# Kernel tuning notes

Measured on AMD Instinct MI355X. Metric: run time of the kernel, lower is better.

## Reference

```python
import jax, jax.numpy as jnp
import numpy as np

NHEAD = 16
EPS = 1e-6

def _phi_norm(x):
    # phi = silu, then L2 normalize over last dim (torch F.normalize: x / max(||x||, eps))
    x = jax.nn.silu(x)
    n = jnp.linalg.norm(x, axis=-1, keepdims=True)
    return x / jnp.maximum(n, EPS)

def setup_inputs() -> dict:
    key = jax.random.key(0)
    k1, k2, k3 = jax.random.split(key, 3)
    B, M, N, D = 4, 1024, 2048, 1024
    q = jax.random.normal(k1, (B, M, D), dtype=jnp.float32)
    kv = jax.random.normal(k2, (B, N, D), dtype=jnp.float32)
    kv_mask = jax.random.bernoulli(k3, 0.1, (B, N))  # True = masked out
    return {"q": q, "kv": kv, "kv_mask": kv_mask}

def reference(q, kv, kv_mask):
    B, M, D = q.shape
    N = kv.shape[1]
    dh = D // NHEAD
    # [B, H, M, dh] / [B, H, N, dh]
    qh = q.reshape(B, M, NHEAD, dh).transpose(0, 2, 1, 3)
    kh = kv.reshape(B, N, NHEAD, dh).transpose(0, 2, 1, 3)
    vh = kh  # values are raw kv heads (no phi/norm)
    qh_n = _phi_norm(qh)
    kh_n = _phi_norm(kh)
    scores = jnp.einsum('bhmd,bhnd->bhmn', qh_n, kh_n) / jnp.sqrt(jnp.asarray(dh, qh_n.dtype))
    scores = jnp.where(kv_mask[:, None, None, :], -jnp.inf, scores)
    attn = jax.nn.softmax(scores.astype(jnp.float32), axis=-1).astype(scores.dtype)
    out = jnp.einsum('bhmn,bhnd->bhmd', attn, vh)
    return out.transpose(0, 2, 1, 3).reshape(B, M, D)
```

## Files before the change

### kernel.cpp

```cpp
#include <hip/hip_runtime.h>
#include <hip/hip_bf16.h>
#include <cmath>
#include <stdint.h>

#define B_ 4
#define M_ 1024
#define N_ 2048
#define D_ 1024
#define H_ 16
#define DH_ 64
#define NT 64
#define NTH 16
#define PITCH 72

typedef __bf16 bf16_t;
typedef __attribute__((ext_vector_type(8))) __bf16 bf16x8;
typedef __attribute__((ext_vector_type(16))) float f32x16;
typedef __attribute__((ext_vector_type(2))) float f32x2;

static __device__ __forceinline__ float silu_f(float x) {
  return x / (1.0f + __expf(-x));
}

static __device__ __forceinline__ unsigned pk2(float a, float b) {
  union { __bf16 h[2]; unsigned u; } p;
  p.h[0] = (__bf16)a; p.h[1] = (__bf16)b;
  return p.u;
}

static __device__ __forceinline__ void gload16(const bf16_t* g, bf16_t* l) {
  typedef __attribute__((address_space(1))) const unsigned GU;
  typedef __attribute__((address_space(3))) unsigned LU;
  __builtin_amdgcn_global_load_lds((GU*)(const unsigned*)g, (LU*)(unsigned*)l,
                                   16, 0, 0);
}

static __device__ __forceinline__ int sw23(int x) {
  return (x & ~12) | ((x & 4) << 1) | ((x & 8) >> 1);
}

__global__ __launch_bounds__(256) void prep_kernel(
    const float* __restrict__ kv, const int* __restrict__ kv_mask,
    bf16_t* __restrict__ kp, bf16_t* __restrict__ vt,
    unsigned long long* __restrict__ mb) {
  __shared__ __align__(16) bf16_t Lt[NT][PITCH];
  const int bx = blockIdx.x;
  const int hp = bx & 7;
  const int nt = (bx >> 3) & 31;
  const int b  = bx >> 8;
  const int n0 = nt * NT;
  const int tid = threadIdx.x;
  const float keep = kv_mask[b * N_ + n0 + (tid >> 2)] ? 0.f : 1.f;

  #pragma unroll
  for (int hi = 0; hi < 2; ++hi) {
    const int h = hp * 2 + hi;
    const size_t bh = (size_t)(b * H_ + h);
    {
      const int r = tid >> 2, c0 = (tid & 3) * 16;
      const float* src = kv + ((size_t)(b * N_ + n0 + r)) * D_ + h * DH_ + c0;
      union { float f[16]; float4 v4[4]; } raw;
      raw.v4[0] = *(const float4*)(src + 0);
      raw.v4[1] = *(const float4*)(src + 4);
      raw.v4[2] = *(const float4*)(src + 8);
      raw.v4[3] = *(const float4*)(src + 12);
      float sv[16];
      float ss = 0.f;
      #pragma unroll
      for (int i = 0; i < 16; ++i) { sv[i] = silu_f(raw.f[i]); ss += sv[i] * sv[i]; }
      ss += __shfl_xor(ss, 1); ss += __shfl_xor(ss, 2);
      const float inv = keep / fmaxf(sqrtf(ss), 1e-6f);
      union { bf16_t bs[16]; uint4 u[2]; } pk;
      #pragma unroll
      for (int i = 0; i < 16; ++i) pk.bs[i] = (bf16_t)(sv[i] * inv);
      uint4* kdst = (uint4*)(kp + (bh * N_ + n0 + r) * DH_ + c0);
      kdst[0] = pk.u[0]; kdst[1] = pk.u[1];
      union { bf16_t bs[16]; uint4 u[2]; } pv;
      #pragma unroll
      for (int i = 0; i < 16; ++i) pv.bs[i] = (bf16_t)(raw.f[i] * keep);
      uint4* ldst = (uint4*)&Lt[r][c0];
      ldst[0] = pv.u[0]; ldst[1] = pv.u[1];
    }
    __syncthreads();
    {
      const int d = tid >> 2, nc = (tid & 3) * 16;
      union { bf16_t bs[16]; uint4 u[2]; } pk;
      #pragma unroll
      for (int i = 0; i < 16; ++i) pk.bs[i] = Lt[nc + i][d];
      uint4* dst = (uint4*)(vt + (bh * DH_ + d) * N_ + n0 + nc);
      dst[0] = pk.u[0]; dst[1] = pk.u[1];
    }
    __syncthreads();
  }
  if (bx == 0 && tid < B_ * (N_ / 64)) {
    const int b2 = tid >> 5, tt = tid & 31;
    unsigned long long m = 0ull;
    for (int i = 0; i < 64; ++i)
      if (kv_mask[b2 * N_ + tt * 64 + i]) m |= (1ull << i);
    mb[tid] = m;
  }
}

__global__ __launch_bounds__(512, 4) void attn_kernel(
    const float* __restrict__ q, const bf16_t* __restrict__ kp,
    const bf16_t* __restrict__ vt, const unsigned long long* __restrict__ mb,
    float* __restrict__ out) {
  __shared__ __align__(1024) char smem[65536];

  const int tid  = threadIdx.x;
  const int w    = tid >> 6;
  const int wq   = w & 3;
  const int half = w >> 2;
  const int lane = tid & 63;
  const int l31  = lane & 31;
  const int hi   = lane >> 5;
  const int rho  = l31 & 7;

  const int wg = (blockIdx.x & 7) * 64 + (blockIdx.x >> 3);
  const int bh = wg >> 3;
  const int m0 = (wg & 7) * 128;
  const int b = bh >> 4, h = bh & 15;

  const bf16_t* kpb = kp + (size_t)bh * N_ * DH_ + (size_t)half * NTH * NT * DH_;
  const bf16_t* vtb = vt + (size_t)bh * DH_ * N_;

  const int srow  = lane >> 3;
  const int sslot = (lane & 7) ^ srow;
  const bf16_t* ks0 = kpb + (size_t)sw23(wq * 16 + srow) * DH_ + sslot * 8;
  const bf16_t* ks1 = kpb + (size_t)sw23(wq * 16 + 8 + srow) * DH_ + sslot * 8;
  const bf16_t* vs0 = vtb + (size_t)(wq * 16 + srow) * N_ + half * NTH * NT + sslot * 8;
  const bf16_t* vs1 = vs0 + 8 * N_;

  {
    bf16_t* Kd = (bf16_t*)(smem + (half * 2 + 0) * 8192) + wq * 16 * DH_;
    bf16_t* Vd = (bf16_t*)(smem + 32768 + (half * 2 + 0) * 8192) + wq * 16 * NT;
    gload16(ks0, Kd); gload16(ks1, Kd + 512);
    gload16(vs0, Vd); gload16(vs1, Vd + 512);
  }

  bf16x8 qb[4];
  {
    const float* qrow =
        q + ((size_t)(b * M_ + m0 + wq * 32 + l31)) * D_ + h * DH_ + hi * 8;
    float sv[32];
    float ss = 0.f;
    #pragma unroll
    for (int kk = 0; kk < 4; ++kk) {
      float4 a0 = *(const float4*)(qrow + kk * 16);
      float4 a1 = *(const float4*)(qrow + kk * 16 + 4);
      sv[kk * 8 + 0] = silu_f(a0.x); sv[kk * 8 + 1] = silu_f(a0.y);
      sv[kk * 8 + 2] = silu_f(a0.z); sv[kk * 8 + 3] = silu_f(a0.w);
      sv[kk * 8 + 4] = silu_f(a1.x); sv[kk * 8 + 5] = silu_f(a1.y);
      sv[kk * 8 + 6] = silu_f(a1.z); sv[kk * 8 + 7] = silu_f(a1.w);
      #pragma unroll
      for (int i = 0; i < 8; ++i) ss += sv[kk * 8 + i] * sv[kk * 8 + i];
    }
    ss += __shfl_xor(ss, 32);
    const float inv = 0.125f / fmaxf(sqrtf(ss), 1e-6f);
    #pragma unroll
    for (int kk = 0; kk < 4; ++kk) {
      union { unsigned u[4]; bf16x8 v; } pq;
      #pragma unroll
      for (int jj = 0; jj < 4; ++jj)
        pq.u[jj] = pk2(sv[kk * 8 + jj * 2] * inv, sv[kk * 8 + jj * 2 + 1] * inv);
      qb[kk] = pq.v;
    }
  }

  int foff[2][4];
  #pragma unroll
  for (int i = 0; i < 2; ++i)
    #pragma unroll
    for (int j = 0; j < 4; ++j)
      foff[i][j] = (i * 32 + l31) * 64 + ((((j << 1) + hi) ^ rho) << 3);

  f32x16 o0, o1, zvec;
  #pragma unroll
  for (int r = 0; r < 16; ++r) { o0[r] = 0.f; o1[r] = 0.f; zvec[r] = 0.f; }
  float lrun = 0.f;
  unsigned cl = 0, ch = 0;
  const unsigned long long* mbb = mb + b * (N_ / 64);

  for (int tt = 0; tt < NTH; ++tt) {
    __syncthreads();
    const int cur = tt & 1;
    if (tt + 1 < NTH) {
      const int nx = cur ^ 1;
      const size_t ko = (size_t)(tt + 1) * NT * DH_;
      const size_t vo = (size_t)(tt + 1) * NT;
      bf16_t* Kd = (bf16_t*)(smem + (half * 2 + nx) * 8192) + wq * 16 * DH_;
      bf16_t* Vd = (bf16_t*)(smem + 32768 + (half * 2 + nx) * 8192) + wq * 16 * NT;
      gload16(ks0 + ko, Kd); gload16(ks1 + ko, Kd + 512);
      gload16(vs0 + vo, Vd); gload16(vs1 + vo, Vd + 512);
    }
    const unsigned long long mk = mbb[half * NTH + tt];
    cl += (unsigned)__popcll(mk & 0x00FF00FF00FF00FFULL);
    ch += (unsigned)__popcll(mk & 0xFF00FF00FF00FF00ULL);

    const bf16_t* Kc = (const bf16_t*)(smem + (half * 2 + cur) * 8192);
    const bf16_t* Vc = (const bf16_t*)(smem + 32768 + (half * 2 + cur) * 8192);

    bf16x8 pa[4];
    #pragma unroll
    for (int nb = 0; nb < 2; ++nb) {
      __builtin_amdgcn_s_setprio(1);
      f32x16 s = __builtin_amdgcn_mfma_f32_32x32x16_bf16(
          *(const bf16x8*)(Kc + foff[nb][0]), qb[0], zvec, 0, 0, 0);
      #pragma unroll
      for (int kk = 1; kk < 4; ++kk) {
        bf16x8 ka = *(const bf16x8*)(Kc + foff[nb][kk]);
        s = __builtin_amdgcn_mfma_f32_32x32x16_bf16(ka, qb[kk], s, 0, 0, 0);
      }
      __builtin_amdgcn_s_setprio(0);

      f32x2 p2[8];
      #pragma unroll
      for (int i = 0; i < 8; ++i) {
        f32x2 x; x.x = s[2 * i]; x.y = s[2 * i + 1];
        f32x2 u = x * 0.5f + 1.0f;
        p2[i] = x * u + 1.0f;
      }
      f32x2 t0 = (p2[0] + p2[1]) + (p2[2] + p2[3]);
      f32x2 t1 = (p2[4] + p2[5]) + (p2[6] + p2[7]);
      f32x2 ts = t0 + t1;
      lrun += ts.x + ts.y;

      union { unsigned u[4]; bf16x8 v; } f0, f1;
      #pragma unroll
      for (int jj = 0; jj < 4; ++jj) {
        f0.u[jj] = pk2(p2[jj].x, p2[jj].y);
        f1.u[jj] = pk2(p2[4 + jj].x, p2[4 + jj].y);
      }
      pa[nb * 2]     = f0.v;
      pa[nb * 2 + 1] = f1.v;
    }

    __builtin_amdgcn_s_setprio(1);
    #pragma unroll
    for (int ks = 0; ks < 4; ++ks) {
      bf16x8 vb0 = *(const bf16x8*)(Vc + foff[0][ks]);
      bf16x8 vb1 = *(const bf16x8*)(Vc + foff[1][ks]);
      o0 = __builtin_amdgcn_mfma_f32_32x32x16_bf16(vb0, pa[ks], o0, 0, 0, 0);
      o1 = __builtin_amdgcn_mfma_f32_32x32x16_bf16(vb1, pa[ks], o1, 0, 0, 0);
    }
    __builtin_amdgcn_s_setprio(0);
  }

  lrun -= (float)(hi ? ch : cl);
  lrun += __shfl_xor(lrun, 32);

  __syncthreads();
  float* Ob = (float*)smem;
  float* Lb = (float*)(smem + 32768);

  if (half == 0) {
    #pragma unroll
    for (int r = 0; r < 16; ++r) {
      const int d = (r & 3) + ((r >> 2) << 3) + (hi << 2);
      Ob[d * 128 + wq * 32 + l31]        = o0[r];
      Ob[(d + 32) * 128 + wq * 32 + l31] = o1[r];
    }
    if (hi == 0) Lb[wq * 32 + l31] = lrun;
  }
  __syncthreads();
  if (half == 1) {
    #pragma unroll
    for (int r = 0; r < 16; ++r) {
      const int d = (r & 3) + ((r >> 2) << 3) + (hi << 2);
      Ob[d * 128 + wq * 32 + l31]        += o0[r];
      Ob[(d + 32) * 128 + wq * 32 + l31] += o1[r];
    }
    if (hi == 0) Lb[wq * 32 + l31] += lrun;
  }
  __syncthreads();
  {
    const int m = tid >> 2, dc = (tid & 3) * 16;
    const float lv = Lb[m];
    const float iv = lv > 0.f ? 1.0f / lv : 0.f;
    float* orow = out + ((size_t)(b * M_ + m0 + m)) * D_ + h * DH_ + dc;
    #pragma unroll
    for (int i0 = 0; i0 < 16; i0 += 4) {
      float4 v;
      v.x = Ob[(dc + i0 + 0) * 128 + m] * iv;
      v.y = Ob[(dc + i0 + 1) * 128 + m] * iv;
      v.z = Ob[(dc + i0 + 2) * 128 + m] * iv;
      v.w = Ob[(dc + i0 + 3) * 128 + m] * iv;
      *(float4*)(orow + i0) = v;
    }
  }
}

extern "C" void kernel_launch(void* const* d_in, const int* in_sizes, int n_in,
                              void* d_out, int out_size, void* d_ws, size_t ws_size,
                              hipStream_t stream) {
  const float* q  = (const float*)d_in[0];
  const float* kv = (const float*)d_in[1];
  const int* kv_mask = (const int*)d_in[2];
  float* out = (float*)d_out;

  bf16_t* kp = (bf16_t*)d_ws;
  bf16_t* vt = kp + (size_t)B_ * H_ * N_ * DH_;
  unsigned long long* mb =
      (unsigned long long*)((char*)d_ws + 2 * (size_t)B_ * H_ * N_ * DH_ * sizeof(bf16_t));

  prep_kernel<<<B_ * 32 * 8, 256, 0, stream>>>(kv, kv_mask, kp, vt, mb);
  attn_kernel<<<B_ * H_ * (M_ / 128), 512, 0, stream>>>(q, kp, vt, mb, out);
}
```

Before: 146.9 us.

## Pre-swizzle K into MFMA fragment layout and load directly to registers

The prep kernel now writes normalized K in a layout matching each lane's MFMA A-operand fragment. The attention kernel loads K straight from global memory into registers, prefetching the next tile during the PV MFMAs, and no longer stages K through LDS. This halves the kernel's shared memory footprint, which may allow more resident workgroups. The cost is more VGPRs for the prefetched fragments and global-load latency exposed inside the loop instead of behind LDS double buffering.

```diff
diff --git a/kernel.cpp b/kernel.cpp
--- a/kernel.cpp
+++ b/kernel.cpp
@@ -73,8 +73,10 @@
       union { bf16_t bs[16]; uint4 u[2]; } pk;
       #pragma unroll
       for (int i = 0; i < 16; ++i) pk.bs[i] = (bf16_t)(sv[i] * inv);
-      uint4* kdst = (uint4*)(kp + (bh * N_ + n0 + r) * DH_ + c0);
-      kdst[0] = pk.u[0]; kdst[1] = pk.u[1];
+      const size_t fbase = bh * 131072 +
+          (size_t)((nt * 8 + (r >> 5) * 4 + (tid & 3)) * 512 + sw23(r & 31) * 8);
+      *(uint4*)(kp + fbase)       = pk.u[0];
+      *(uint4*)(kp + fbase + 256) = pk.u[1];
       union { bf16_t bs[16]; uint4 u[2]; } pv;
       #pragma unroll
       for (int i = 0; i < 16; ++i) pv.bs[i] = (bf16_t)(raw.f[i] * keep);
@@ -105,7 +107,7 @@
     const float* __restrict__ q, const bf16_t* __restrict__ kp,
     const bf16_t* __restrict__ vt, const unsigned long long* __restrict__ mb,
     float* __restrict__ out) {
-  __shared__ __align__(1024) char smem[65536];
+  __shared__ __align__(1024) char smem[33280];
 
   const int tid  = threadIdx.x;
   const int w    = tid >> 6;
@@ -121,22 +123,25 @@
   const int m0 = (wg & 7) * 128;
   const int b = bh >> 4, h = bh & 15;
 
-  const bf16_t* kpb = kp + (size_t)bh * N_ * DH_ + (size_t)half * NTH * NT * DH_;
   const bf16_t* vtb = vt + (size_t)bh * DH_ * N_;
+  const bf16_t* kfb = kp + (size_t)bh * 131072 + (size_t)half * 65536
+                         + (size_t)lane * 8;
 
   const int srow  = lane >> 3;
   const int sslot = (lane & 7) ^ srow;
-  const bf16_t* ks0 = kpb + (size_t)sw23(wq * 16 + srow) * DH_ + sslot * 8;
-  const bf16_t* ks1 = kpb + (size_t)sw23(wq * 16 + 8 + srow) * DH_ + sslot * 8;
   const bf16_t* vs0 = vtb + (size_t)(wq * 16 + srow) * N_ + half * NTH * NT + sslot * 8;
   const bf16_t* vs1 = vs0 + 8 * N_;
 
   {
-    bf16_t* Kd = (bf16_t*)(smem + (half * 2 + 0) * 8192) + wq * 16 * DH_;
-    bf16_t* Vd = (bf16_t*)(smem + 32768 + (half * 2 + 0) * 8192) + wq * 16 * NT;
-    gload16(ks0, Kd); gload16(ks1, Kd + 512);
+    bf16_t* Vd = (bf16_t*)(smem + (half * 2 + 0) * 8192) + wq * 16 * NT;
     gload16(vs0, Vd); gload16(vs1, Vd + 512);
   }
+  bf16x8 ka[2][4];
+  #pragma unroll
+  for (int nb = 0; nb < 2; ++nb)
+    #pragma unroll
+    for (int kk = 0; kk < 4; ++kk)
+      ka[nb][kk] = *(const bf16x8*)(kfb + (nb * 4 + kk) * 512);
 
   bf16x8 qb[4];
   {
@@ -186,31 +191,25 @@
     const int cur = tt & 1;
     if (tt + 1 < NTH) {
       const int nx = cur ^ 1;
-      const size_t ko = (size_t)(tt + 1) * NT * DH_;
       const size_t vo = (size_t)(tt + 1) * NT;
-      bf16_t* Kd = (bf16_t*)(smem + (half * 2 + nx) * 8192) + wq * 16 * DH_;
-      bf16_t* Vd = (bf16_t*)(smem + 32768 + (half * 2 + nx) * 8192) + wq * 16 * NT;
-      gload16(ks0 + ko, Kd); gload16(ks1 + ko, Kd + 512);
+      bf16_t* Vd = (bf16_t*)(smem + (half * 2 + nx) * 8192) + wq * 16 * NT;
       gload16(vs0 + vo, Vd); gload16(vs1 + vo, Vd + 512);
     }
     const unsigned long long mk = mbb[half * NTH + tt];
     cl += (unsigned)__popcll(mk & 0x00FF00FF00FF00FFULL);
     ch += (unsigned)__popcll(mk & 0xFF00FF00FF00FF00ULL);
 
-    const bf16_t* Kc = (const bf16_t*)(smem + (half * 2 + cur) * 8192);
-    const bf16_t* Vc = (const bf16_t*)(smem + 32768 + (half * 2 + cur) * 8192);
+    const bf16_t* Vc = (const bf16_t*)(smem + (half * 2 + cur) * 8192);
 
     bf16x8 pa[4];
     #pragma unroll
     for (int nb = 0; nb < 2; ++nb) {
       __builtin_amdgcn_s_setprio(1);
       f32x16 s = __builtin_amdgcn_mfma_f32_32x32x16_bf16(
-          *(const bf16x8*)(Kc + foff[nb][0]), qb[0], zvec, 0, 0, 0);
-      #pragma unroll
-      for (int kk = 1; kk < 4; ++kk) {
-        bf16x8 ka = *(const bf16x8*)(Kc + foff[nb][kk]);
-        s = __builtin_amdgcn_mfma_f32_32x32x16_bf16(ka, qb[kk], s, 0, 0, 0);
-      }
+          ka[nb][0], qb[0], zvec, 0, 0, 0);
+      #pragma unroll
+      for (int kk = 1; kk < 4; ++kk)
+        s = __builtin_amdgcn_mfma_f32_32x32x16_bf16(ka[nb][kk], qb[kk], s, 0, 0, 0);
       __builtin_amdgcn_s_setprio(0);
 
       f32x2 p2[8];
@@ -235,6 +234,15 @@
       pa[nb * 2 + 1] = f1.v;
     }
 
+    {
+      const bf16_t* kn = kfb + (size_t)((tt + 1) & 15) * 4096;
+      #pragma unroll
+      for (int nb = 0; nb < 2; ++nb)
+        #pragma unroll
+        for (int kk = 0; kk < 4; ++kk)
+          ka[nb][kk] = *(const bf16x8*)(kn + (nb * 4 + kk) * 512);
+    }
+
     __builtin_amdgcn_s_setprio(1);
     #pragma unroll
     for (int ks = 0; ks < 4; ++ks) {
```

After: 142.7 us. 1.03x faster.
